# Kernel optimization log

Measured on AMD Instinct MI355X. Metric: run time of the kernel, lower is better.

Reference implementation:

```python
import jax, jax.numpy as jnp
import numpy as np

D_K = 128
SCALER = np.sqrt(D_K).astype(np.float32)

def setup_inputs() -> dict:
    key = jax.random.key(0)
    kq, kk, kv = jax.random.split(key, 3)
    B, L, D = 16, 2048, D_K
    q = jax.random.normal(kq, (B, L, D), dtype=jnp.float32)
    k = jax.random.normal(kk, (B, L, D), dtype=jnp.float32)
    v = jax.random.normal(kv, (B, L, D), dtype=jnp.float32)
    return {"q": q, "k": k, "v": v}

def reference(q, k, v):
    # score[b, i, j] = q[b, i, :] . k[b, j, :] / sqrt(d_k)
    score = jnp.einsum('bid,bjd->bij', q, k) / SCALER
    attn = jax.nn.softmax(score, axis=-1)
    # output[b, i, :] = sum_j attn[b, i, j] * v[b, j, :]
    return jnp.einsum('bij,bjd->bid', attn, v)
```

## Files before the change

kernel.cpp:

```cpp
#include <hip/hip_runtime.h>
#include <stdint.h>


typedef short bf16x8 __attribute__((ext_vector_type(8)));
typedef float f32x4 __attribute__((ext_vector_type(4)));

#define L_SEQ  2048
#define D_HEAD 128
#define TKV    64
#define NIT    (L_SEQ / TKV)
#define KST    136
#define VST    72
#define PST    72
#define OST    132

#define K_OFF  0
#define V_OFF  17408
#define P_OFF  (17408 + 18432)
#define SMEM_BYTES (P_OFF + 4*32*PST*2)

__device__ __forceinline__ unsigned pk2(float lo, float hi) {
    union { float f; unsigned u; } a, b;
    a.f = lo; b.f = hi;
    return __builtin_amdgcn_perm(b.u + 0x8000u, a.u + 0x8000u, 0x07060302u);
}
__device__ __forceinline__ float ex2(float x) { return __builtin_amdgcn_exp2f(x); }

union F4 { float4 v; float f[4]; };

__global__ __launch_bounds__(256, 1)
void attn_fwd(const float* __restrict__ Qg, const float* __restrict__ Kg,
              const float* __restrict__ Vg, float* __restrict__ Og) {
    __shared__ __align__(16) char smem[SMEM_BYTES];
    unsigned short* Kl = (unsigned short*)(smem + K_OFF);
    unsigned short* Vl = (unsigned short*)(smem + V_OFF);
    float*          Ol = (float*)smem;

    const int tid  = threadIdx.x;
    const int wv   = tid >> 6;
    const int lane = tid & 63;
    const int c    = lane & 15;
    const int qd   = lane >> 4;
    unsigned short* Pl = (unsigned short*)(smem + P_OFF) + wv * (32 * PST);

    const int b  = blockIdx.x & 15;
    const int qb = blockIdx.x >> 4;

    const float* Qb = Qg + (size_t)b * L_SEQ * D_HEAD;
    const float* Kb = Kg + (size_t)b * L_SEQ * D_HEAD;
    const float* Vb = Vg + (size_t)b * L_SEQ * D_HEAD;

    const int krow = tid >> 2, kch = tid & 3;
    const int vcc  = tid & 31, vgk = tid >> 5;

    const float QS = 1.4426950408889634f / 11.313708498984761f;
    bf16x8 qf[2][4];
    #pragma unroll
    for (int s = 0; s < 2; ++s) {
        const float* qrow = Qb + (size_t)(qb * 128 + wv * 32 + s * 16 + c) * D_HEAD + qd * 8;
        #pragma unroll
        for (int kt = 0; kt < 4; ++kt) {
            float4 x0 = *(const float4*)(qrow + kt * 32);
            float4 x1 = *(const float4*)(qrow + kt * 32 + 4);
            union { unsigned u[4]; bf16x8 v; } t;
            t.u[0] = pk2(x0.x * QS, x0.y * QS);
            t.u[1] = pk2(x0.z * QS, x0.w * QS);
            t.u[2] = pk2(x1.x * QS, x1.y * QS);
            t.u[3] = pk2(x1.z * QS, x1.w * QS);
            qf[s][kt] = t.v;
        }
    }

    F4 kreg[8], vreg[8];
    {
        const float* kp = Kb + (size_t)krow * D_HEAD + kch * 32;
        #pragma unroll
        for (int r = 0; r < 8; ++r) kreg[r].v = *(const float4*)(kp + r * 4);
        const float* vp = Vb + (size_t)(vgk * 8) * D_HEAD + vcc * 4;
        #pragma unroll
        for (int r = 0; r < 8; ++r) vreg[r].v = *(const float4*)(vp + (size_t)r * D_HEAD);
    }

    f32x4 acc[2][8];
    #pragma unroll
    for (int s = 0; s < 2; ++s)
        #pragma unroll
        for (int dt = 0; dt < 8; ++dt) acc[s][dt] = (f32x4){0.f, 0.f, 0.f, 0.f};
    float lrun[2] = {0.f, 0.f};

    for (int it = 0; it < NIT; ++it) {
        #pragma unroll
        for (int i = 0; i < 4; ++i) {
            uint4 w;
            w.x = pk2(kreg[2*i].f[0],   kreg[2*i].f[1]);
            w.y = pk2(kreg[2*i].f[2],   kreg[2*i].f[3]);
            w.z = pk2(kreg[2*i+1].f[0], kreg[2*i+1].f[1]);
            w.w = pk2(kreg[2*i+1].f[2], kreg[2*i+1].f[3]);
            *(uint4*)(&Kl[krow * KST + kch * 32 + i * 8]) = w;
        }
        #pragma unroll
        for (int dd = 0; dd < 4; ++dd) {
            uint4 w;
            w.x = pk2(vreg[0].f[dd], vreg[1].f[dd]);
            w.y = pk2(vreg[2].f[dd], vreg[3].f[dd]);
            w.z = pk2(vreg[4].f[dd], vreg[5].f[dd]);
            w.w = pk2(vreg[6].f[dd], vreg[7].f[dd]);
            *(uint4*)(&Vl[(vcc * 4 + dd) * VST + vgk * 8]) = w;
        }
        __syncthreads();

        if (it + 1 < NIT) {
            const float* kp = Kb + (size_t)((it + 1) * TKV + krow) * D_HEAD + kch * 32;
            #pragma unroll
            for (int r = 0; r < 8; ++r) kreg[r].v = *(const float4*)(kp + r * 4);
            const float* vp = Vb + (size_t)((it + 1) * TKV + vgk * 8) * D_HEAD + vcc * 4;
            #pragma unroll
            for (int r = 0; r < 8; ++r) vreg[r].v = *(const float4*)(vp + (size_t)r * D_HEAD);
        }

        f32x4 st[4][2];
        #pragma unroll
        for (int v = 0; v < 4; ++v) { st[v][0] = (f32x4){0,0,0,0}; st[v][1] = (f32x4){0,0,0,0}; }
        #pragma unroll
        for (int kt = 0; kt < 4; ++kt) {
            #pragma unroll
            for (int v = 0; v < 4; ++v) {
                bf16x8 a = *(const bf16x8*)(&Kl[(v * 16 + c) * KST + kt * 32 + qd * 8]);
                st[v][0] = __builtin_amdgcn_mfma_f32_16x16x32_bf16(a, qf[0][kt], st[v][0], 0, 0, 0);
                st[v][1] = __builtin_amdgcn_mfma_f32_16x16x32_bf16(a, qf[1][kt], st[v][1], 0, 0, 0);
            }
        }

        #pragma unroll
        for (int s = 0; s < 2; ++s) {
            float lsum = 0.f;
            #pragma unroll
            for (int v = 0; v < 4; ++v) {
                float p0 = ex2(st[v][s].x), p1 = ex2(st[v][s].y);
                float p2 = ex2(st[v][s].z), p3 = ex2(st[v][s].w);
                lsum += (p0 + p1) + (p2 + p3);
                uint2 w; w.x = pk2(p0, p1); w.y = pk2(p2, p3);
                *(uint2*)(&Pl[(s * 16 + c) * PST + v * 16 + qd * 4]) = w;
            }
            lrun[s] += lsum;
        }
        bf16x8 pf[2][2];
        #pragma unroll
        for (int h = 0; h < 2; ++h)
            #pragma unroll
            for (int s = 0; s < 2; ++s)
                pf[h][s] = *(const bf16x8*)(&Pl[(s * 16 + c) * PST + h * 32 + qd * 8]);

        #pragma unroll
        for (int dt = 0; dt < 8; ++dt) {
            #pragma unroll
            for (int h = 0; h < 2; ++h) {
                bf16x8 a = *(const bf16x8*)(&Vl[(dt * 16 + c) * VST + h * 32 + qd * 8]);
                acc[0][dt] = __builtin_amdgcn_mfma_f32_16x16x32_bf16(a, pf[h][0], acc[0][dt], 0, 0, 0);
                acc[1][dt] = __builtin_amdgcn_mfma_f32_16x16x32_bf16(a, pf[h][1], acc[1][dt], 0, 0, 0);
            }
        }
        __syncthreads();
    }

    float inv[2];
    #pragma unroll
    for (int s = 0; s < 2; ++s) {
        float l = lrun[s];
        l += __shfl_xor(l, 16);
        l += __shfl_xor(l, 32);
        inv[s] = 1.0f / l;
    }
    #pragma unroll
    for (int pass = 0; pass < 2; ++pass) {
        if ((wv >> 1) == pass) {
            int rw = (wv & 1) * 32;
            #pragma unroll
            for (int s = 0; s < 2; ++s)
                #pragma unroll
                for (int dt = 0; dt < 8; ++dt) {
                    f32x4 o = acc[s][dt];
                    float4 w = {o.x * inv[s], o.y * inv[s], o.z * inv[s], o.w * inv[s]};
                    *(float4*)(&Ol[(rw + s * 16 + c) * OST + dt * 16 + qd * 4]) = w;
                }
        }
        __syncthreads();
        #pragma unroll
        for (int i = 0; i < 8; ++i) {
            int idx = i * 256 + tid;
            int row = idx >> 5, c4 = idx & 31;
            float4 val = *(const float4*)(&Ol[row * OST + c4 * 4]);
            size_t q = (size_t)b * L_SEQ + qb * 128 + pass * 64 + row;
            *(float4*)(Og + q * D_HEAD + c4 * 4) = val;
        }
        __syncthreads();
    }
}

extern "C" void kernel_launch(void* const* d_in, const int* in_sizes, int n_in,
                              void* d_out, int out_size, void* d_ws, size_t ws_size,
                              hipStream_t stream) {
    const float* q = (const float*)d_in[0];
    const float* k = (const float*)d_in[1];
    const float* v = (const float*)d_in[2];
    float* out = (float*)d_out;
    dim3 grid(256), block(256);
    attn_fwd<<<grid, block, 0, stream>>>(q, k, v, out);
}
```

Before: 166.3 us.

## Pre-convert K/V to swizzled bf16 in workspace and stream via direct-to-LDS loads

```diff
diff --git a/kernel.cpp b/kernel.cpp
--- a/kernel.cpp
+++ b/kernel.cpp
@@ -4,20 +4,13 @@
 
 typedef short bf16x8 __attribute__((ext_vector_type(8)));
 typedef float f32x4 __attribute__((ext_vector_type(4)));
+typedef unsigned int u32;
+typedef unsigned short u16;
 
 #define L_SEQ  2048
 #define D_HEAD 128
-#define TKV    64
-#define NIT    (L_SEQ / TKV)
-#define KST    136
-#define VST    72
-#define PST    72
-#define OST    132
-
-#define K_OFF  0
-#define V_OFF  17408
-#define P_OFF  (17408 + 18432)
-#define SMEM_BYTES (P_OFF + 4*32*PST*2)
+#define NIT    32
+#define TSZ    (16u * 2048u * 128u * 2u)
 
 __device__ __forceinline__ unsigned pk2(float lo, float hi) {
     union { float f; unsigned u; } a, b;
@@ -25,15 +18,225 @@
     return __builtin_amdgcn_perm(b.u + 0x8000u, a.u + 0x8000u, 0x07060302u);
 }
 __device__ __forceinline__ float ex2(float x) { return __builtin_amdgcn_exp2f(x); }
-
-union F4 { float4 v; float f[4]; };
+__device__ __forceinline__ void gl_lds16(const u16* g, u16* l) {
+    __builtin_amdgcn_global_load_lds(
+        (const __attribute__((address_space(1))) u32*)g,
+        (__attribute__((address_space(3))) u32*)l, 16, 0, 0);
+}
+
+__global__ __launch_bounds__(256, 4)
+void prepass(const float* __restrict__ K, const float* __restrict__ V,
+             u16* __restrict__ kb, u16* __restrict__ vt) {
+    const int id = blockIdx.x, t = threadIdx.x;
+    if (id < 512) {
+        const float* src = K + (size_t)id * 64 * 128;
+        u16*        dst = kb + (size_t)id * 64 * 128;
+        const int r = t >> 2;
+        #pragma unroll
+        for (int i = 0; i < 4; ++i) {
+            int gp = (t & 3) * 4 + i;
+            int gs = gp ^ (r & 7);
+            const float* s = src + r * 128 + gs * 8;
+            float4 x0 = *(const float4*)s, x1 = *(const float4*)(s + 4);
+            uint4 w;
+            w.x = pk2(x0.x, x0.y); w.y = pk2(x0.z, x0.w);
+            w.z = pk2(x1.x, x1.y); w.w = pk2(x1.z, x1.w);
+            *(uint4*)(dst + r * 128 + gp * 8) = w;
+        }
+    } else {
+        __shared__ float vl[64 * 132];
+        const int bid = id - 512;
+        const float* src = V + (size_t)bid * 64 * 128;
+        {
+            int r = t >> 2, c0 = (t & 3) * 32;
+            #pragma unroll
+            for (int j = 0; j < 8; ++j)
+                *(float4*)(&vl[r * 132 + c0 + j * 4]) =
+                    *(const float4*)(src + r * 128 + c0 + j * 4);
+        }
+        __syncthreads();
+        u16* dst = vt + (size_t)bid * 8192;
+        const int d = t >> 1;
+        #pragma unroll
+        for (int i = 0; i < 4; ++i) {
+            int gp = (t & 1) * 4 + i;
+            int kvb = (gp ^ (d & 7)) * 8;
+            float p[8];
+            #pragma unroll
+            for (int j = 0; j < 8; ++j) p[j] = vl[(kvb + j) * 132 + d];
+            uint4 w;
+            w.x = pk2(p[0], p[1]); w.y = pk2(p[2], p[3]);
+            w.z = pk2(p[4], p[5]); w.w = pk2(p[6], p[7]);
+            *(uint4*)(dst + d * 64 + gp * 8) = w;
+        }
+    }
+}
 
 __global__ __launch_bounds__(256, 1)
-void attn_fwd(const float* __restrict__ Qg, const float* __restrict__ Kg,
-              const float* __restrict__ Vg, float* __restrict__ Og) {
-    __shared__ __align__(16) char smem[SMEM_BYTES];
-    unsigned short* Kl = (unsigned short*)(smem + K_OFF);
-    unsigned short* Vl = (unsigned short*)(smem + V_OFF);
+void attn_fwd(const float* __restrict__ Qg, const u16* __restrict__ kb,
+              const u16* __restrict__ vt, float* __restrict__ Og) {
+    __shared__ __align__(16) char smem[51200];
+    const int tid = threadIdx.x;
+    const int wv = tid >> 6, lane = tid & 63;
+    const int c = lane & 15, qd = lane >> 4, cx = c & 7;
+    const int b = blockIdx.x & 15, qblk = blockIdx.x >> 4;
+
+    const float* Qp = Qg + (size_t)b * L_SEQ * D_HEAD;
+    const u16*   Kp = kb + (size_t)b * L_SEQ * D_HEAD;
+    const u16*   Vp = vt + (size_t)b * 32 * 8192;
+    u16* Kl = (u16*)smem;
+    u16* Vl = (u16*)(smem + 16384);
+    u16* Pl = (u16*)(smem + 32768) + wv * 2304;
+
+    const int so = wv * 2048 + lane * 8;
+
+    #pragma unroll
+    for (int i = 0; i < 4; ++i) {
+        gl_lds16(Kp + so + i * 512, Kl + so + i * 512);
+        gl_lds16(Vp + so + i * 512, Vl + so + i * 512);
+    }
+
+    const float QS = 1.4426950408889634f / 11.313708498984761f;
+    bf16x8 qf[2][4];
+    #pragma unroll
+    for (int s = 0; s < 2; ++s) {
+        const float* qrow = Qp + (size_t)(qblk * 128 + wv * 32 + s * 16 + c) * 128 + qd * 8;
+        #pragma unroll
+        for (int kt = 0; kt < 4; ++kt) {
+            float4 x0 = *(const float4*)(qrow + kt * 32);
+            float4 x1 = *(const float4*)(qrow + kt * 32 + 4);
+            union { unsigned u[4]; bf16x8 v; } tt;
+            tt.u[0] = pk2(x0.x * QS, x0.y * QS);
+            tt.u[1] = pk2(x0.z * QS, x0.w * QS);
+            tt.u[2] = pk2(x1.x * QS, x1.y * QS);
+            tt.u[3] = pk2(x1.z * QS, x1.w * QS);
+            qf[s][kt] = tt.v;
+        }
+    }
+
+    f32x4 acc[2][8];
+    #pragma unroll
+    for (int s = 0; s < 2; ++s)
+        #pragma unroll
+        for (int dt = 0; dt < 8; ++dt) acc[s][dt] = (f32x4){0.f, 0.f, 0.f, 0.f};
+    float lrun[2] = {0.f, 0.f};
+
+    __syncthreads();
+
+    for (int it = 0; it < NIT; ++it) {
+        f32x4 st[4][2];
+        #pragma unroll
+        for (int v = 0; v < 4; ++v) {
+            st[v][0] = (f32x4){0.f, 0.f, 0.f, 0.f};
+            st[v][1] = (f32x4){0.f, 0.f, 0.f, 0.f};
+        }
+        #pragma unroll
+        for (int kt = 0; kt < 4; ++kt) {
+            const int g = ((kt * 4 + qd) ^ cx) * 8;
+            #pragma unroll
+            for (int v = 0; v < 4; ++v) {
+                bf16x8 a = *(const bf16x8*)(Kl + (v * 16 + c) * 128 + g);
+                st[v][0] = __builtin_amdgcn_mfma_f32_16x16x32_bf16(a, qf[0][kt], st[v][0], 0, 0, 0);
+                st[v][1] = __builtin_amdgcn_mfma_f32_16x16x32_bf16(a, qf[1][kt], st[v][1], 0, 0, 0);
+            }
+        }
+        __syncthreads();
+
+        if (it + 1 < NIT) {
+            const u16* kg = Kp + (size_t)(it + 1) * 8192 + so;
+            #pragma unroll
+            for (int i = 0; i < 4; ++i) gl_lds16(kg + i * 512, Kl + so + i * 512);
+        }
+
+        #pragma unroll
+        for (int s = 0; s < 2; ++s) {
+            float lsum = 0.f;
+            #pragma unroll
+            for (int v = 0; v < 4; ++v) {
+                float p0 = ex2(st[v][s].x), p1 = ex2(st[v][s].y);
+                float p2 = ex2(st[v][s].z), p3 = ex2(st[v][s].w);
+                lsum += (p0 + p1) + (p2 + p3);
+                uint2 w; w.x = pk2(p0, p1); w.y = pk2(p2, p3);
+                *(uint2*)(Pl + (s * 16 + c) * 72 + v * 16 + qd * 4) = w;
+            }
+            lrun[s] += lsum;
+        }
+        bf16x8 pf[2][2];
+        #pragma unroll
+        for (int h = 0; h < 2; ++h)
+            #pragma unroll
+            for (int s = 0; s < 2; ++s)
+                pf[h][s] = *(const bf16x8*)(Pl + (s * 16 + c) * 72 + h * 32 + qd * 8);
+
+        #pragma unroll
+        for (int dt = 0; dt < 8; ++dt) {
+            #pragma unroll
+            for (int h = 0; h < 2; ++h) {
+                bf16x8 a = *(const bf16x8*)(Vl + (dt * 16 + c) * 64 + ((h * 4 + qd) ^ cx) * 8);
+                acc[0][dt] = __builtin_amdgcn_mfma_f32_16x16x32_bf16(a, pf[h][0], acc[0][dt], 0, 0, 0);
+                acc[1][dt] = __builtin_amdgcn_mfma_f32_16x16x32_bf16(a, pf[h][1], acc[1][dt], 0, 0, 0);
+            }
+        }
+        __syncthreads();
+
+        if (it + 1 < NIT) {
+            const u16* vg = Vp + (size_t)(it + 1) * 8192 + so;
+            #pragma unroll
+            for (int i = 0; i < 4; ++i) gl_lds16(vg + i * 512, Vl + so + i * 512);
+        }
+    }
+
+    float inv[2];
+    #pragma unroll
+    for (int s = 0; s < 2; ++s) {
+        float l = lrun[s];
+        l += __shfl_xor(l, 16);
+        l += __shfl_xor(l, 32);
+        inv[s] = 1.0f / l;
+    }
+    float* Ol = (float*)smem;
+    #pragma unroll
+    for (int pass = 0; pass < 2; ++pass) {
+        if ((wv >> 1) == pass) {
+            int rw = (wv & 1) * 32;
+            #pragma unroll
+            for (int s = 0; s < 2; ++s)
+                #pragma unroll
+                for (int dt = 0; dt < 8; ++dt) {
+                    f32x4 o = acc[s][dt];
+                    float4 w = {o.x * inv[s], o.y * inv[s], o.z * inv[s], o.w * inv[s]};
+                    *(float4*)(&Ol[(rw + s * 16 + c) * 132 + dt * 16 + qd * 4]) = w;
+                }
+        }
+        __syncthreads();
+        #pragma unroll
+        for (int i = 0; i < 8; ++i) {
+            int idx = i * 256 + tid;
+            int row = idx >> 5, c4 = idx & 31;
+            float4 val = *(const float4*)(&Ol[row * 132 + c4 * 4]);
+            size_t q = (size_t)b * L_SEQ + qblk * 128 + pass * 64 + row;
+            *(float4*)(Og + q * D_HEAD + c4 * 4) = val;
+        }
+        __syncthreads();
+    }
+}
+
+#define FKST 136
+#define FVST 72
+#define FPST 72
+#define FOST 132
+#define FV_OFF  17408
+#define FP_OFF  (17408 + 18432)
+#define FSMEM   (FP_OFF + 4 * 32 * FPST * 2)
+
+union F4fb { float4 v; float f[4]; };
+
+__global__ __launch_bounds__(256, 1)
+void attn_fwd_fb(const float* __restrict__ Qg, const float* __restrict__ Kg,
+                 const float* __restrict__ Vg, float* __restrict__ Og) {
+    __shared__ __align__(16) char smem[FSMEM];
+    unsigned short* Kl = (unsigned short*)(smem);
+    unsigned short* Vl = (unsigned short*)(smem + FV_OFF);
     float*          Ol = (float*)smem;
 
     const int tid  = threadIdx.x;
@@ -41,7 +244,7 @@
     const int lane = tid & 63;
     const int c    = lane & 15;
     const int qd   = lane >> 4;
-    unsigned short* Pl = (unsigned short*)(smem + P_OFF) + wv * (32 * PST);
+    unsigned short* Pl = (unsigned short*)(smem + FP_OFF) + wv * (32 * FPST);
 
     const int b  = blockIdx.x & 15;
     const int qb = blockIdx.x >> 4;
@@ -71,7 +274,7 @@
         }
     }
 
-    F4 kreg[8], vreg[8];
+    F4fb kreg[8], vreg[8];
     {
         const float* kp = Kb + (size_t)krow * D_HEAD + kch * 32;
         #pragma unroll
@@ -88,7 +291,7 @@
         for (int dt = 0; dt < 8; ++dt) acc[s][dt] = (f32x4){0.f, 0.f, 0.f, 0.f};
     float lrun[2] = {0.f, 0.f};
 
-    for (int it = 0; it < NIT; ++it) {
+    for (int it = 0; it < 32; ++it) {
         #pragma unroll
         for (int i = 0; i < 4; ++i) {
             uint4 w;
@@ -96,7 +299,7 @@
             w.y = pk2(kreg[2*i].f[2],   kreg[2*i].f[3]);
             w.z = pk2(kreg[2*i+1].f[0], kreg[2*i+1].f[1]);
             w.w = pk2(kreg[2*i+1].f[2], kreg[2*i+1].f[3]);
-            *(uint4*)(&Kl[krow * KST + kch * 32 + i * 8]) = w;
+            *(uint4*)(&Kl[krow * FKST + kch * 32 + i * 8]) = w;
         }
         #pragma unroll
         for (int dd = 0; dd < 4; ++dd) {
@@ -105,15 +308,15 @@
             w.y = pk2(vreg[2].f[dd], vreg[3].f[dd]);
             w.z = pk2(vreg[4].f[dd], vreg[5].f[dd]);
             w.w = pk2(vreg[6].f[dd], vreg[7].f[dd]);
-            *(uint4*)(&Vl[(vcc * 4 + dd) * VST + vgk * 8]) = w;
-        }
-        __syncthreads();
-
-        if (it + 1 < NIT) {
-            const float* kp = Kb + (size_t)((it + 1) * TKV + krow) * D_HEAD + kch * 32;
+            *(uint4*)(&Vl[(vcc * 4 + dd) * FVST + vgk * 8]) = w;
+        }
+        __syncthreads();
+
+        if (it + 1 < 32) {
+            const float* kp = Kb + (size_t)((it + 1) * 64 + krow) * D_HEAD + kch * 32;
             #pragma unroll
             for (int r = 0; r < 8; ++r) kreg[r].v = *(const float4*)(kp + r * 4);
-            const float* vp = Vb + (size_t)((it + 1) * TKV + vgk * 8) * D_HEAD + vcc * 4;
+            const float* vp = Vb + (size_t)((it + 1) * 64 + vgk * 8) * D_HEAD + vcc * 4;
             #pragma unroll
             for (int r = 0; r < 8; ++r) vreg[r].v = *(const float4*)(vp + (size_t)r * D_HEAD);
         }
@@ -125,7 +328,7 @@
         for (int kt = 0; kt < 4; ++kt) {
             #pragma unroll
             for (int v = 0; v < 4; ++v) {
-                bf16x8 a = *(const bf16x8*)(&Kl[(v * 16 + c) * KST + kt * 32 + qd * 8]);
+                bf16x8 a = *(const bf16x8*)(&Kl[(v * 16 + c) * FKST + kt * 32 + qd * 8]);
                 st[v][0] = __builtin_amdgcn_mfma_f32_16x16x32_bf16(a, qf[0][kt], st[v][0], 0, 0, 0);
                 st[v][1] = __builtin_amdgcn_mfma_f32_16x16x32_bf16(a, qf[1][kt], st[v][1], 0, 0, 0);
             }
@@ -140,7 +343,7 @@
                 float p2 = ex2(st[v][s].z), p3 = ex2(st[v][s].w);
                 lsum += (p0 + p1) + (p2 + p3);
                 uint2 w; w.x = pk2(p0, p1); w.y = pk2(p2, p3);
-                *(uint2*)(&Pl[(s * 16 + c) * PST + v * 16 + qd * 4]) = w;
+                *(uint2*)(&Pl[(s * 16 + c) * FPST + v * 16 + qd * 4]) = w;
             }
             lrun[s] += lsum;
         }
@@ -149,13 +352,13 @@
         for (int h = 0; h < 2; ++h)
             #pragma unroll
             for (int s = 0; s < 2; ++s)
-                pf[h][s] = *(const bf16x8*)(&Pl[(s * 16 + c) * PST + h * 32 + qd * 8]);
+                pf[h][s] = *(const bf16x8*)(&Pl[(s * 16 + c) * FPST + h * 32 + qd * 8]);
 
         #pragma unroll
         for (int dt = 0; dt < 8; ++dt) {
             #pragma unroll
             for (int h = 0; h < 2; ++h) {
-                bf16x8 a = *(const bf16x8*)(&Vl[(dt * 16 + c) * VST + h * 32 + qd * 8]);
+                bf16x8 a = *(const bf16x8*)(&Vl[(dt * 16 + c) * FVST + h * 32 + qd * 8]);
                 acc[0][dt] = __builtin_amdgcn_mfma_f32_16x16x32_bf16(a, pf[h][0], acc[0][dt], 0, 0, 0);
                 acc[1][dt] = __builtin_amdgcn_mfma_f32_16x16x32_bf16(a, pf[h][1], acc[1][dt], 0, 0, 0);
             }
@@ -181,7 +384,7 @@
                 for (int dt = 0; dt < 8; ++dt) {
                     f32x4 o = acc[s][dt];
                     float4 w = {o.x * inv[s], o.y * inv[s], o.z * inv[s], o.w * inv[s]};
-                    *(float4*)(&Ol[(rw + s * 16 + c) * OST + dt * 16 + qd * 4]) = w;
+                    *(float4*)(&Ol[(rw + s * 16 + c) * FOST + dt * 16 + qd * 4]) = w;
                 }
         }
         __syncthreads();
@@ -189,7 +392,7 @@
         for (int i = 0; i < 8; ++i) {
             int idx = i * 256 + tid;
             int row = idx >> 5, c4 = idx & 31;
-            float4 val = *(const float4*)(&Ol[row * OST + c4 * 4]);
+            float4 val = *(const float4*)(&Ol[row * FOST + c4 * 4]);
             size_t q = (size_t)b * L_SEQ + qb * 128 + pass * 64 + row;
             *(float4*)(Og + q * D_HEAD + c4 * 4) = val;
         }
@@ -204,6 +407,12 @@
     const float* k = (const float*)d_in[1];
     const float* v = (const float*)d_in[2];
     float* out = (float*)d_out;
-    dim3 grid(256), block(256);
-    attn_fwd<<<grid, block, 0, stream>>>(q, k, v, out);
-}
+    if (ws_size >= (size_t)(2u * TSZ)) {
+        u16* kb = (u16*)d_ws;
+        u16* vt = (u16*)((char*)d_ws + TSZ);
+        prepass<<<dim3(1024), dim3(256), 0, stream>>>(k, v, kb, vt);
+        attn_fwd<<<dim3(256), dim3(256), 0, stream>>>(q, kb, vt, out);
+    } else {
+        attn_fwd_fb<<<dim3(256), dim3(256), 0, stream>>>(q, k, v, out);
+    }
+}
```

Result: faster. 161.7 us (-2.8%).
